# Performance work log

Measured on AMD Instinct MI355X. Metric: run time of the kernel, lower is better.

Reference implementation:

```python
import jax, jax.numpy as jnp
import numpy as np

EPS = 1e-8

def setup_inputs() -> dict:
    key = jax.random.key(0)
    ks = jax.random.split(key, 12)
    bsz, input_dim, output_dim = 65536, 512, 512
    base_mem_size, category_mem_size, mem_dim, n_cat = 100, 5, 64, 35
    def kaiming(k, shape):
        fan_in = shape[-1]
        bound = np.sqrt(6.0 / fan_in)  # kaiming_uniform with a=sqrt(5) default gain approximated by gain=1 uniform: sqrt(6/fan_in)
        return jax.random.uniform(k, shape, jnp.float32, -bound, bound)
    def linear(kw, kb, out_d, in_d):
        bound = 1.0 / np.sqrt(in_d)
        W = jax.random.uniform(kw, (out_d, in_d), jnp.float32, -bound, bound)
        b = jax.random.uniform(kb, (out_d,), jnp.float32, -bound, bound)
        return W, b
    W_base, b_base = linear(ks[0], ks[1], mem_dim, input_dim)
    W_cat, b_cat = linear(ks[2], ks[3], mem_dim, input_dim)
    W_out, b_out = linear(ks[4], ks[5], output_dim, 2 * mem_dim)
    base_keys = kaiming(ks[6], (base_mem_size, mem_dim))
    base_vals = kaiming(ks[7], (base_mem_size, mem_dim))
    cat_keys = kaiming(ks[8], (n_cat, category_mem_size, mem_dim))
    cat_vals = kaiming(ks[9], (n_cat, category_mem_size, mem_dim))
    query = jax.random.normal(ks[10], (bsz, input_dim), jnp.float32)
    category_idxs = jax.random.randint(ks[11], (bsz,), 0, n_cat)
    return {"query": query, "category_idxs": category_idxs,
            "W_base": W_base, "b_base": b_base, "W_cat": W_cat, "b_cat": b_cat,
            "base_keys": base_keys, "base_vals": base_vals,
            "cat_keys": cat_keys, "cat_vals": cat_vals,
            "W_out": W_out, "b_out": b_out}

def _l2norm(x, axis=-1):
    n = jnp.sqrt(jnp.sum(x * x, axis=axis, keepdims=True))
    return x / jnp.maximum(n, EPS)

def reference(query, category_idxs, W_base, b_base, W_cat, b_cat,
              base_keys, base_vals, cat_keys, cat_vals, W_out, b_out):
    # --- base memory lookup (cosine sim + softmax + weighted sum) ---
    base_query = query @ W_base.T + b_base                      # [b, d]
    base_sims = _l2norm(base_query) @ _l2norm(base_keys).T      # [b, M]
    base_attn = jax.nn.softmax(base_sims, axis=-1)
    base_lookup = base_attn @ base_vals                         # [b, d]
    # --- category memory lookup (gather + dot + softmax + weighted sum) ---
    cat_query = query @ W_cat.T + b_cat                         # [b, d]
    ck = cat_keys[category_idxs]                                # [b, K, d]
    cv = cat_vals[category_idxs]                                # [b, K, d]
    cat_sims = jnp.einsum('bd,bkd->bk', cat_query, ck)          # [b, K]
    cat_attn = jax.nn.softmax(cat_sims, axis=-1)
    cat_lookup = jnp.einsum('bk,bkd->bd', cat_attn, cv)         # [b, d]
    # --- output projection ---
    combined = jnp.concatenate([base_lookup, cat_lookup], axis=1)  # [b, 2d]
    return combined @ W_out.T + b_out                           # [b, out]
```

## Files before the change

kernel.cpp:

```cpp
#include <hip/hip_runtime.h>

typedef _Float16 f16;
typedef _Float16 f16x4 __attribute__((ext_vector_type(4)));
typedef _Float16 f16x8 __attribute__((ext_vector_type(8)));
typedef float    f32x4 __attribute__((ext_vector_type(4)));

#define BATCH 65536
#define INDIM 512
#define MD    64
#define MSZ   100
#define NCAT  35
#define CKSZ  5
#define ODIM  512
#define N1    256
#define K2    128
#define NSLOT (NCAT*CKSZ)
#define RBS   232

static __device__ __forceinline__ f32x4 mfma16(f16x4 a, f16x4 b, f32x4 c) {
  return __builtin_amdgcn_mfma_f32_16x16x16f16(a, b, c, 0, 0, 0);
}

#define GLD_LDS16(g, l)                                                        \
  __builtin_amdgcn_global_load_lds(                                            \
      (const __attribute__((address_space(1))) void*)(g),                      \
      (__attribute__((address_space(3))) void*)(l), 16, 0, 0)

__global__ __launch_bounds__(256) void k_prep(
    const float* __restrict__ Wb, const float* __restrict__ bb,
    const float* __restrict__ Wc, const float* __restrict__ bc,
    const float* __restrict__ keys, const float* __restrict__ bvals,
    const float* __restrict__ cvals, const float* __restrict__ Wo,
    f16* __restrict__ B1p, float* __restrict__ bias1,
    f16* __restrict__ B2p, f16* __restrict__ C2cat) {
  int id = blockIdx.x * 256 + threadIdx.x;
  if (id < 32768) {
    int l = id & 63, ntile = id >> 11;
    int n = ntile * 16 + (l & 15);
    int kb = ((id >> 6) & 31) * 16 + 4 * (l >> 4);
    float v0 = 0.f, v1 = 0.f, v2 = 0.f, v3 = 0.f;
    if (n < 64) {
      const float* w = Wb + n * INDIM + kb;
      v0 = w[0]; v1 = w[1]; v2 = w[2]; v3 = w[3];
    } else if (n < 128) {
      const float* w = Wc + (n - 64) * INDIM + kb;
      v0 = w[0]; v1 = w[1]; v2 = w[2]; v3 = w[3];
    } else if (n < 128 + MSZ) {
      int m = n - 128;
      float ss = 0.f;
      for (int d = 0; d < MD; d++) { float kv = keys[m * MD + d]; ss += kv * kv; }
      float rin = 1.f / fmaxf(sqrtf(ss), 1e-8f);
      for (int d = 0; d < MD; d++) {
        float kd = keys[m * MD + d];
        const float* wr = Wb + d * INDIM + kb;
        v0 += wr[0] * kd; v1 += wr[1] * kd; v2 += wr[2] * kd; v3 += wr[3] * kd;
      }
      v0 *= rin; v1 *= rin; v2 *= rin; v3 *= rin;
    }
    f16x4 o; o[0] = (f16)v0; o[1] = (f16)v1; o[2] = (f16)v2; o[3] = (f16)v3;
    *(f16x4*)(B1p + (size_t)id * 4) = o;
  } else if (id < 49152) {
    int q2 = id - 32768;
    int l = q2 & 63, otile = q2 >> 9;
    int o = otile * 16 + (l & 15);
    int kkb = ((q2 >> 6) & 7) * 16 + 4 * (l >> 4);
    float v0 = 0.f, v1 = 0.f, v2 = 0.f, v3 = 0.f;
    if (kkb < MSZ) {
      for (int d = 0; d < MD; d++) {
        float w = Wo[o * 128 + d];
        v0 += bvals[(kkb + 0) * MD + d] * w;
        v1 += bvals[(kkb + 1) * MD + d] * w;
        v2 += bvals[(kkb + 2) * MD + d] * w;
        v3 += bvals[(kkb + 3) * MD + d] * w;
      }
    }
    f16x4 o4; o4[0] = (f16)v0; o4[1] = (f16)v1; o4[2] = (f16)v2; o4[3] = (f16)v3;
    *(f16x4*)(B2p + (size_t)q2 * 4) = o4;
  } else if (id < 138752) {
    int id3 = id - 49152;
    int s = id3 >> 9, o = id3 & 511;
    float a = 0.f;
    for (int d = 0; d < MD; d++) a += cvals[s * MD + d] * Wo[o * 128 + 64 + d];
    C2cat[(size_t)s * ODIM + o] = (f16)a;
  } else if (id < 139008) {
    int n = id - 138752;
    float bv = 0.f;
    if (n < 64) bv = bb[n];
    else if (n < 128) bv = bc[n - 64];
    else if (n < 128 + MSZ) {
      int m = n - 128;
      float ss = 0.f;
      for (int d = 0; d < MD; d++) { float kv = keys[m * MD + d]; ss += kv * kv; }
      float rin = 1.f / fmaxf(sqrtf(ss), 1e-8f);
      float a = 0.f;
      for (int d = 0; d < MD; d++) a += bb[d] * keys[m * MD + d];
      bv = a * rin;
    }
    bias1[n] = bv;
  }
}

__global__ __launch_bounds__(512) void k_g1mid(const float* __restrict__ q,
    const f16* __restrict__ B1p, const float* __restrict__ bias1,
    const int* __restrict__ cidx, const float* __restrict__ catk,
    f16* __restrict__ A2, float* __restrict__ cwg, int* __restrict__ csg) {
  __shared__ __align__(16) char smem[128 * RBS * 2];
  f16 (*Al)[72] = (f16(*)[72])smem;
  f16* BlF = (f16*)(smem + 18432);
  char* BlB = smem + 18432;
  f16 (*rb)[RBS] = (f16(*)[RBS])smem;

  const int tid = threadIdx.x;
  const int lane = tid & 63, wid = tid >> 6;
  const int wm = wid & 1, wn = wid >> 1;
  const int row0 = blockIdx.x * 128;
  const int l15 = lane & 15, l4 = lane >> 4;
  f32x4 acc[4][4];
#pragma unroll
  for (int i = 0; i < 4; i++)
#pragma unroll
    for (int j = 0; j < 4; j++) acc[i][j] = (f32x4){0.f, 0.f, 0.f, 0.f};

  const int arow = tid >> 2, aseg = tid & 3;
  const char* B1pB = (const char*)B1p;

  for (int k0 = 0; k0 < INDIM; k0 += 64) {
    const float* qp = q + (size_t)(row0 + arow) * INDIM + k0 + aseg * 16;
    f32x4 a0 = *(const f32x4*)qp;
    f32x4 a1 = *(const f32x4*)(qp + 4);
    f32x4 a2 = *(const f32x4*)(qp + 8);
    f32x4 a3 = *(const f32x4*)(qp + 12);
    f16x8 av0, av1;
#pragma unroll
    for (int i = 0; i < 4; i++) { av0[i] = (f16)a0[i]; av0[4 + i] = (f16)a1[i]; }
#pragma unroll
    for (int i = 0; i < 4; i++) { av1[i] = (f16)a2[i]; av1[4 + i] = (f16)a3[i]; }
    __syncthreads();
    {
      const int ksoff = (k0 >> 4) * 512;
#pragma unroll
      for (int c = 0; c < 4; c++) {
        const int t = wid * 2 + (c >> 1), h = (c & 1) * 1024;
        GLD_LDS16(B1pB + (size_t)t * 16384 + ksoff + h + lane * 16,
                  BlB + t * 2048 + h);
      }
    }
    *(f16x8*)&Al[arow][aseg * 16]     = av0;
    *(f16x8*)&Al[arow][aseg * 16 + 8] = av1;
    __syncthreads();
#pragma unroll
    for (int kk = 0; kk < 4; kk++) {
      const int kc = kk * 16 + 4 * l4;
      f16x4 af[4], bf[4];
#pragma unroll
      for (int mi = 0; mi < 4; mi++) af[mi] = *(const f16x4*)&Al[wm * 64 + mi * 16 + l15][kc];
#pragma unroll
      for (int ni = 0; ni < 4; ni++)
        bf[ni] = *(const f16x4*)(BlF + ((size_t)(wn * 4 + ni) * 4 + kk) * 256 + lane * 4);
#pragma unroll
      for (int mi = 0; mi < 4; mi++)
#pragma unroll
        for (int ni = 0; ni < 4; ni++)
          acc[mi][ni] = mfma16(af[mi], bf[ni], acc[mi][ni]);
    }
  }
  __syncthreads();

#pragma unroll
  for (int ni = 0; ni < 4; ni++) {
    const int col = wn * 64 + ni * 16 + l15;
    const float bs = bias1[col];
    if (col < RBS) {
#pragma unroll
      for (int mi = 0; mi < 4; mi++) {
        const int r = wm * 64 + mi * 16 + 4 * l4;
#pragma unroll
        for (int j = 0; j < 4; j++)
          rb[r + j][col] = (f16)(acc[mi][ni][j] + bs);
      }
    }
  }
  __syncthreads();

  {
    const int row = tid >> 2, s = tid & 3;
    f16x8 v0 = *(const f16x8*)&rb[row][s * 16];
    f16x8 v1 = *(const f16x8*)&rb[row][s * 16 + 8];
    float nb = 0.f;
#pragma unroll
    for (int i = 0; i < 8; i++) { float x = (float)v0[i]; nb += x * x; }
#pragma unroll
    for (int i = 0; i < 8; i++) { float x = (float)v1[i]; nb += x * x; }
    nb += __shfl_xor(nb, 1, 64);
    nb += __shfl_xor(nb, 2, 64);
    const float rinv = 1.f / fmaxf(sqrtf(nb), 1e-8f);

    float sv[25];
#pragma unroll
    for (int i = 0; i < 25; i++)
      sv[i] = (float)rb[row][128 + s * 25 + i] * rinv;
    float mx = sv[0];
#pragma unroll
    for (int i = 1; i < 25; i++) mx = fmaxf(mx, sv[i]);
    mx = fmaxf(mx, __shfl_xor(mx, 1, 64));
    mx = fmaxf(mx, __shfl_xor(mx, 2, 64));
    float es = 0.f;
#pragma unroll
    for (int i = 0; i < 25; i++) { sv[i] = __expf(sv[i] - mx); es += sv[i]; }
    es += __shfl_xor(es, 1, 64);
    es += __shfl_xor(es, 2, 64);
    const float isum = 1.f / es;

    const int ci = cidx[row0 + row];
    const float* kp = catk + (size_t)ci * (CKSZ * MD) + s * 16;
    f16x8 c0 = *(const f16x8*)&rb[row][64 + s * 16];
    f16x8 c1 = *(const f16x8*)&rb[row][64 + s * 16 + 8];
    float cqf[16];
#pragma unroll
    for (int i = 0; i < 8; i++) { cqf[i] = (float)c0[i]; cqf[8 + i] = (float)c1[i]; }
    float t[5];
#pragma unroll
    for (int sl = 0; sl < 5; sl++) {
      f32x4 k0 = *(const f32x4*)(kp + sl * MD);
      f32x4 k1 = *(const f32x4*)(kp + sl * MD + 4);
      f32x4 k2 = *(const f32x4*)(kp + sl * MD + 8);
      f32x4 k3 = *(const f32x4*)(kp + sl * MD + 12);
      float a = 0.f;
#pragma unroll
      for (int i = 0; i < 4; i++) a += cqf[i] * k0[i];
#pragma unroll
      for (int i = 0; i < 4; i++) a += cqf[4 + i] * k1[i];
#pragma unroll
      for (int i = 0; i < 4; i++) a += cqf[8 + i] * k2[i];
#pragma unroll
      for (int i = 0; i < 4; i++) a += cqf[12 + i] * k3[i];
      a += __shfl_xor(a, 1, 64);
      a += __shfl_xor(a, 2, 64);
      t[sl] = a;
    }

#pragma unroll
    for (int i = 0; i < 25; i++)
      rb[row][128 + s * 25 + i] = (f16)(sv[i] * isum);

    if (s == 0) {
      float m5 = fmaxf(fmaxf(fmaxf(t[0], t[1]), fmaxf(t[2], t[3])), t[4]);
      float e0 = __expf(t[0] - m5), e1 = __expf(t[1] - m5), e2 = __expf(t[2] - m5),
            e3 = __expf(t[3] - m5), e4 = __expf(t[4] - m5);
      float ics = 1.f / (e0 + e1 + e2 + e3 + e4);
      float* cwr = cwg + (size_t)(row0 + row) * 5;
      cwr[0] = e0 * ics; cwr[1] = e1 * ics; cwr[2] = e2 * ics;
      cwr[3] = e3 * ics; cwr[4] = e4 * ics;
      csg[row0 + row] = ci * CKSZ;
    }
  }
  __syncthreads();

  {
    const int row = tid >> 2, s = tid & 3;
    f16 tmp[32];
#pragma unroll
    for (int i = 0; i < 32; i++) {
      const int k = s * 32 + i;
      tmp[i] = (k < MSZ) ? rb[row][128 + k] : (f16)0.f;
    }
    f16* dst = A2 + (size_t)(row0 + row) * K2 + s * 32;
#pragma unroll
    for (int i = 0; i < 4; i++)
      *(f16x8*)(dst + i * 8) = *(const f16x8*)&tmp[i * 8];
  }
}

__global__ __launch_bounds__(512) void k_gemm2(const f16* __restrict__ A2,
    const f16* __restrict__ B2p, const float* __restrict__ cwg,
    const int* __restrict__ csg, const f16* __restrict__ C2cat,
    const float* __restrict__ bout, float* __restrict__ out) {
  __shared__ f16 As[128][136];
  __shared__ float cws[128][5];
  __shared__ int csi[128];
  const int tid = threadIdx.x;
  const int lane = tid & 63, wid = tid >> 6;
  const int wm = wid & 1, wn = wid >> 1;
  const int l15 = lane & 15, l4 = lane >> 4;
  const int row0 = blockIdx.x * 128;
  const int col0 = blockIdx.y * 256;

  {
    const int r = tid >> 2, seg = tid & 3;
    const f16* src = A2 + (size_t)(row0 + r) * K2 + seg * 32;
#pragma unroll
    for (int i = 0; i < 4; i++)
      *(f16x8*)&As[r][seg * 32 + i * 8] = *(const f16x8*)(src + i * 8);
  }
  if (tid < 128) {
#pragma unroll
    for (int i = 0; i < 5; i++) cws[tid][i] = cwg[(size_t)(row0 + tid) * 5 + i];
    csi[tid] = csg[row0 + tid];
  }
  __syncthreads();

  f32x4 acc[4][4];
#pragma unroll
  for (int i = 0; i < 4; i++)
#pragma unroll
    for (int j = 0; j < 4; j++) acc[i][j] = (f32x4){0.f, 0.f, 0.f, 0.f};

#pragma unroll
  for (int ks = 0; ks < 8; ks++) {
    f16x4 af[4], bf[4];
#pragma unroll
    for (int mi = 0; mi < 4; mi++)
      af[mi] = *(const f16x4*)&As[wm * 64 + mi * 16 + l15][ks * 16 + 4 * l4];
#pragma unroll
    for (int ni = 0; ni < 4; ni++)
      bf[ni] = *(const f16x4*)(B2p +
        (((size_t)(blockIdx.y * 16 + wn * 4 + ni) * 8 + ks) * 64 + lane) * 4);
#pragma unroll
    for (int mi = 0; mi < 4; mi++)
#pragma unroll
      for (int ni = 0; ni < 4; ni++)
        acc[mi][ni] = mfma16(af[mi], bf[ni], acc[mi][ni]);
  }

  float bs[4];
#pragma unroll
  for (int ni = 0; ni < 4; ni++) bs[ni] = bout[col0 + wn * 64 + ni * 16 + l15];
#pragma unroll
  for (int mi = 0; mi < 4; mi++) {
#pragma unroll
    for (int j = 0; j < 4; j++) {
      const int r = wm * 64 + mi * 16 + 4 * l4 + j;
      const int cb = csi[r];
      const float w0 = cws[r][0], w1 = cws[r][1], w2 = cws[r][2],
                  w3 = cws[r][3], w4 = cws[r][4];
      const f16* cp = C2cat + (size_t)cb * ODIM + col0 + wn * 64 + l15;
#pragma unroll
      for (int ni = 0; ni < 4; ni++) {
        const int col = col0 + wn * 64 + ni * 16 + l15;
        const f16* cpn = cp + ni * 16;
        float v = acc[mi][ni][j] + bs[ni];
        v += w0 * (float)cpn[0]
           + w1 * (float)cpn[ODIM]
           + w2 * (float)cpn[2 * ODIM]
           + w3 * (float)cpn[3 * ODIM]
           + w4 * (float)cpn[4 * ODIM];
        out[(size_t)(row0 + r) * ODIM + col] = v;
      }
    }
  }
}

extern "C" void kernel_launch(void* const* d_in, const int* in_sizes, int n_in,
                              void* d_out, int out_size, void* d_ws, size_t ws_size,
                              hipStream_t stream) {
  const float* query = (const float*)d_in[0];
  const int*   cidx  = (const int*)d_in[1];
  const float* Wb    = (const float*)d_in[2];
  const float* bb    = (const float*)d_in[3];
  const float* Wc    = (const float*)d_in[4];
  const float* bc    = (const float*)d_in[5];
  const float* bkeys = (const float*)d_in[6];
  const float* bvals = (const float*)d_in[7];
  const float* ckeys = (const float*)d_in[8];
  const float* cvals = (const float*)d_in[9];
  const float* Wo    = (const float*)d_in[10];
  const float* bo    = (const float*)d_in[11];
  float* out = (float*)d_out;

  char* ws = (char*)d_ws;
  f16*   A2    = (f16*)(ws);
  float* cwg   = (float*)(ws + 16777216);
  int*   csg   = (int*)(ws + 18087936);
  f16*   B1p   = (f16*)(ws + 18350080);
  f16*   B2p   = (f16*)(ws + 18612224);
  f16*   C2cat = (f16*)(ws + 18743296);
  float* bias1 = (float*)(ws + 18922496);

  k_prep<<<dim3((139008 + 255) / 256), 256, 0, stream>>>(
      Wb, bb, Wc, bc, bkeys, bvals, cvals, Wo, B1p, bias1, B2p, C2cat);
  k_g1mid<<<dim3(BATCH / 128), 512, 0, stream>>>(
      query, B1p, bias1, cidx, ckeys, A2, cwg, csg);
  k_gemm2<<<dim3(BATCH / 128, 2), 512, 0, stream>>>(A2, B2p, cwg, csg, C2cat, bo, out);
}
```

Baseline: 107.6 us.

## Compute category lookup in mid kernel and fold into output GEMM K dimension

The category softmax-weighted value sum is now computed in the first kernel and written as 64 extra columns of A2, so the output GEMM runs with K=192 using raw W_out columns. This removes the per-element gather of precomputed category-value projections and the weight/index buffers in the epilogue, along with the large C2cat precompute. In exchange, A2 traffic grows by half and the GEMM does 50% more MFMA work.

```diff
diff --git a/kernel.cpp b/kernel.cpp
--- a/kernel.cpp
+++ b/kernel.cpp
@@ -13,8 +13,7 @@
 #define CKSZ  5
 #define ODIM  512
 #define N1    256
-#define K2    128
-#define NSLOT (NCAT*CKSZ)
+#define K2    192
 #define RBS   232
 
 static __device__ __forceinline__ f32x4 mfma16(f16x4 a, f16x4 b, f32x4 c) {
@@ -30,9 +29,8 @@
     const float* __restrict__ Wb, const float* __restrict__ bb,
     const float* __restrict__ Wc, const float* __restrict__ bc,
     const float* __restrict__ keys, const float* __restrict__ bvals,
-    const float* __restrict__ cvals, const float* __restrict__ Wo,
-    f16* __restrict__ B1p, float* __restrict__ bias1,
-    f16* __restrict__ B2p, f16* __restrict__ C2cat) {
+    const float* __restrict__ Wo,
+    f16* __restrict__ B1p, float* __restrict__ bias1, f16* __restrict__ B2p) {
   int id = blockIdx.x * 256 + threadIdx.x;
   if (id < 32768) {
     int l = id & 63, ntile = id >> 11;
@@ -59,11 +57,13 @@
     }
     f16x4 o; o[0] = (f16)v0; o[1] = (f16)v1; o[2] = (f16)v2; o[3] = (f16)v3;
     *(f16x4*)(B1p + (size_t)id * 4) = o;
-  } else if (id < 49152) {
+  } else if (id < 57344) {
     int q2 = id - 32768;
-    int l = q2 & 63, otile = q2 >> 9;
+    int otile = q2 / 768;
+    int rem = q2 - otile * 768;
+    int ks = rem >> 6, l = rem & 63;
     int o = otile * 16 + (l & 15);
-    int kkb = ((q2 >> 6) & 7) * 16 + 4 * (l >> 4);
+    int kkb = ks * 16 + 4 * (l >> 4);
     float v0 = 0.f, v1 = 0.f, v2 = 0.f, v3 = 0.f;
     if (kkb < MSZ) {
       for (int d = 0; d < MD; d++) {
@@ -73,17 +73,14 @@
         v2 += bvals[(kkb + 2) * MD + d] * w;
         v3 += bvals[(kkb + 3) * MD + d] * w;
       }
+    } else if (kkb >= 128) {
+      const float* w = Wo + o * 128 + (kkb - 64);
+      v0 = w[0]; v1 = w[1]; v2 = w[2]; v3 = w[3];
     }
     f16x4 o4; o4[0] = (f16)v0; o4[1] = (f16)v1; o4[2] = (f16)v2; o4[3] = (f16)v3;
     *(f16x4*)(B2p + (size_t)q2 * 4) = o4;
-  } else if (id < 138752) {
-    int id3 = id - 49152;
-    int s = id3 >> 9, o = id3 & 511;
-    float a = 0.f;
-    for (int d = 0; d < MD; d++) a += cvals[s * MD + d] * Wo[o * 128 + 64 + d];
-    C2cat[(size_t)s * ODIM + o] = (f16)a;
-  } else if (id < 139008) {
-    int n = id - 138752;
+  } else if (id < 57600) {
+    int n = id - 57344;
     float bv = 0.f;
     if (n < 64) bv = bb[n];
     else if (n < 128) bv = bc[n - 64];
@@ -103,7 +100,7 @@
 __global__ __launch_bounds__(512) void k_g1mid(const float* __restrict__ q,
     const f16* __restrict__ B1p, const float* __restrict__ bias1,
     const int* __restrict__ cidx, const float* __restrict__ catk,
-    f16* __restrict__ A2, float* __restrict__ cwg, int* __restrict__ csg) {
+    const float* __restrict__ cvals, f16* __restrict__ A2) {
   __shared__ __align__(16) char smem[128 * RBS * 2];
   f16 (*Al)[72] = (f16(*)[72])smem;
   f16* BlF = (f16*)(smem + 18432);
@@ -243,16 +240,37 @@
     for (int i = 0; i < 25; i++)
       rb[row][128 + s * 25 + i] = (f16)(sv[i] * isum);
 
-    if (s == 0) {
-      float m5 = fmaxf(fmaxf(fmaxf(t[0], t[1]), fmaxf(t[2], t[3])), t[4]);
-      float e0 = __expf(t[0] - m5), e1 = __expf(t[1] - m5), e2 = __expf(t[2] - m5),
-            e3 = __expf(t[3] - m5), e4 = __expf(t[4] - m5);
-      float ics = 1.f / (e0 + e1 + e2 + e3 + e4);
-      float* cwr = cwg + (size_t)(row0 + row) * 5;
-      cwr[0] = e0 * ics; cwr[1] = e1 * ics; cwr[2] = e2 * ics;
-      cwr[3] = e3 * ics; cwr[4] = e4 * ics;
-      csg[row0 + row] = ci * CKSZ;
-    }
+    float m5 = fmaxf(fmaxf(fmaxf(t[0], t[1]), fmaxf(t[2], t[3])), t[4]);
+    float e0 = __expf(t[0] - m5), e1 = __expf(t[1] - m5), e2 = __expf(t[2] - m5),
+          e3 = __expf(t[3] - m5), e4 = __expf(t[4] - m5);
+    const float ics = 1.f / (e0 + e1 + e2 + e3 + e4);
+    float wv[5] = {e0 * ics, e1 * ics, e2 * ics, e3 * ics, e4 * ics};
+
+    const float* vb = cvals + (size_t)(ci * CKSZ) * MD + s * 16;
+    float cv[16];
+#pragma unroll
+    for (int i = 0; i < 16; i++) cv[i] = 0.f;
+#pragma unroll
+    for (int sl = 0; sl < 5; sl++) {
+      f32x4 u0 = *(const f32x4*)(vb + sl * MD);
+      f32x4 u1 = *(const f32x4*)(vb + sl * MD + 4);
+      f32x4 u2 = *(const f32x4*)(vb + sl * MD + 8);
+      f32x4 u3 = *(const f32x4*)(vb + sl * MD + 12);
+      const float w = wv[sl];
+#pragma unroll
+      for (int i = 0; i < 4; i++) {
+        cv[i]      += w * u0[i];
+        cv[4 + i]  += w * u1[i];
+        cv[8 + i]  += w * u2[i];
+        cv[12 + i] += w * u3[i];
+      }
+    }
+    f16x8 ch0, ch1;
+#pragma unroll
+    for (int i = 0; i < 8; i++) { ch0[i] = (f16)cv[i]; ch1[i] = (f16)cv[8 + i]; }
+    f16* cdst = A2 + (size_t)(row0 + row) * K2 + 128 + s * 16;
+    *(f16x8*)cdst = ch0;
+    *(f16x8*)(cdst + 8) = ch1;
   }
   __syncthreads();
 
@@ -272,12 +290,9 @@
 }
 
 __global__ __launch_bounds__(512) void k_gemm2(const f16* __restrict__ A2,
-    const f16* __restrict__ B2p, const float* __restrict__ cwg,
-    const int* __restrict__ csg, const f16* __restrict__ C2cat,
-    const float* __restrict__ bout, float* __restrict__ out) {
-  __shared__ f16 As[128][136];
-  __shared__ float cws[128][5];
-  __shared__ int csi[128];
+    const f16* __restrict__ B2p, const float* __restrict__ bout,
+    float* __restrict__ out) {
+  __shared__ f16 As[128][200];
   const int tid = threadIdx.x;
   const int lane = tid & 63, wid = tid >> 6;
   const int wm = wid & 1, wn = wid >> 1;
@@ -287,15 +302,10 @@
 
   {
     const int r = tid >> 2, seg = tid & 3;
-    const f16* src = A2 + (size_t)(row0 + r) * K2 + seg * 32;
-#pragma unroll
-    for (int i = 0; i < 4; i++)
-      *(f16x8*)&As[r][seg * 32 + i * 8] = *(const f16x8*)(src + i * 8);
-  }
-  if (tid < 128) {
-#pragma unroll
-    for (int i = 0; i < 5; i++) cws[tid][i] = cwg[(size_t)(row0 + tid) * 5 + i];
-    csi[tid] = csg[row0 + tid];
+    const f16* src = A2 + (size_t)(row0 + r) * K2 + seg * 48;
+#pragma unroll
+    for (int i = 0; i < 6; i++)
+      *(f16x8*)&As[r][seg * 48 + i * 8] = *(const f16x8*)(src + i * 8);
   }
   __syncthreads();
 
@@ -306,7 +316,7 @@
     for (int j = 0; j < 4; j++) acc[i][j] = (f32x4){0.f, 0.f, 0.f, 0.f};
 
 #pragma unroll
-  for (int ks = 0; ks < 8; ks++) {
+  for (int ks = 0; ks < 12; ks++) {
     f16x4 af[4], bf[4];
 #pragma unroll
     for (int mi = 0; mi < 4; mi++)
@@ -314,7 +324,7 @@
 #pragma unroll
     for (int ni = 0; ni < 4; ni++)
       bf[ni] = *(const f16x4*)(B2p +
-        (((size_t)(blockIdx.y * 16 + wn * 4 + ni) * 8 + ks) * 64 + lane) * 4);
+        (((size_t)(blockIdx.y * 16 + wn * 4 + ni) * 12 + ks) * 64 + lane) * 4);
 #pragma unroll
     for (int mi = 0; mi < 4; mi++)
 #pragma unroll
@@ -330,21 +340,10 @@
 #pragma unroll
     for (int j = 0; j < 4; j++) {
       const int r = wm * 64 + mi * 16 + 4 * l4 + j;
-      const int cb = csi[r];
-      const float w0 = cws[r][0], w1 = cws[r][1], w2 = cws[r][2],
-                  w3 = cws[r][3], w4 = cws[r][4];
-      const f16* cp = C2cat + (size_t)cb * ODIM + col0 + wn * 64 + l15;
 #pragma unroll
       for (int ni = 0; ni < 4; ni++) {
         const int col = col0 + wn * 64 + ni * 16 + l15;
-        const f16* cpn = cp + ni * 16;
-        float v = acc[mi][ni][j] + bs[ni];
-        v += w0 * (float)cpn[0]
-           + w1 * (float)cpn[ODIM]
-           + w2 * (float)cpn[2 * ODIM]
-           + w3 * (float)cpn[3 * ODIM]
-           + w4 * (float)cpn[4 * ODIM];
-        out[(size_t)(row0 + r) * ODIM + col] = v;
+        out[(size_t)(row0 + r) * ODIM + col] = acc[mi][ni][j] + bs[ni];
       }
     }
   }
@@ -369,16 +368,13 @@
 
   char* ws = (char*)d_ws;
   f16*   A2    = (f16*)(ws);
-  float* cwg   = (float*)(ws + 16777216);
-  int*   csg   = (int*)(ws + 18087936);
-  f16*   B1p   = (f16*)(ws + 18350080);
-  f16*   B2p   = (f16*)(ws + 18612224);
-  f16*   C2cat = (f16*)(ws + 18743296);
-  float* bias1 = (float*)(ws + 18922496);
-
-  k_prep<<<dim3((139008 + 255) / 256), 256, 0, stream>>>(
-      Wb, bb, Wc, bc, bkeys, bvals, cvals, Wo, B1p, bias1, B2p, C2cat);
+  f16*   B1p   = (f16*)(ws + 25165824);
+  f16*   B2p   = (f16*)(ws + 25427968);
+  float* bias1 = (float*)(ws + 25624576);
+
+  k_prep<<<dim3(57600 / 256), 256, 0, stream>>>(
+      Wb, bb, Wc, bc, bkeys, bvals, Wo, B1p, bias1, B2p);
   k_g1mid<<<dim3(BATCH / 128), 512, 0, stream>>>(
-      query, B1p, bias1, cidx, ckeys, A2, cwg, csg);
-  k_gemm2<<<dim3(BATCH / 128, 2), 512, 0, stream>>>(A2, B2p, cwg, csg, C2cat, bo, out);
-}
+      query, B1p, bias1, cidx, ckeys, cvals, A2);
+  k_gemm2<<<dim3(BATCH / 128, 2), 512, 0, stream>>>(A2, B2p, bo, out);
+}
```

New measurement: 101.2 us. 1.06x faster.
